# Kernel tuning notes

Hardware: AMD Instinct MI355X
Metric: run time of the kernel (lower is better)

The kernel has to match this reference:

```python
import jax, jax.numpy as jnp
import numpy as np

B, N, C = 256, 196, 768
H, HD = 12, 64          # num_heads, head_dim
WS = 14                 # window side, N = WS*WS
EPS = 1e-6


def setup_inputs() -> dict:
    key = jax.random.key(0)
    ks = jax.random.split(key, 7)
    s = 0.02
    return {
        "x": jax.random.normal(ks[0], (B, N, C), jnp.float32),
        "w_qkv": jax.random.normal(ks[1], (C, 3 * C), jnp.float32) * s,
        "pos_enc": jax.random.normal(ks[2], (1, N, C), jnp.float32) * s,
        "dwc_w": jax.random.normal(ks[3], (HD, 1, 5, 5), jnp.float32) * s,
        "dwc_b": jax.random.normal(ks[4], (HD,), jnp.float32) * s,
        "w_proj": jax.random.normal(ks[5], (C, C), jnp.float32) * s,
        "b_proj": jax.random.normal(ks[6], (C,), jnp.float32) * s,
    }


def _heads(t):
    # (B, N, C) -> (B*H, N, HD)   ['b n (h c) -> (b h) n c']
    return t.reshape(B, N, H, HD).transpose(0, 2, 1, 3).reshape(B * H, N, HD)


def reference(x, w_qkv, pos_enc, dwc_w, dwc_b, w_proj, b_proj):
    qkv = (x @ w_qkv).reshape(B, N, 3, C)
    q, k, v = qkv[:, :, 0], qkv[:, :, 1], qkv[:, :, 2]
    k = k + pos_enc
    # ReLU kernel feature map
    q = jax.nn.relu(q)
    k = jax.nn.relu(k)
    q, k, v = _heads(q), _heads(k), _heads(v)          # (BH, N, HD) each, fp32
    # normalizer z_i = 1 / (q_i . sum_j k_j + eps)
    z = 1.0 / (jnp.einsum("bic,bc->bi", q, k.sum(axis=1)) + EPS)
    # kv-first order (i*j*(c+d) > c*d*(i+j) for N=196, HD=64)
    kv = jnp.einsum("bjc,bjd->bcd", k, v)              # (BH, HD, HD)
    out = jnp.einsum("bic,bcd,bi->bid", q, kv, z)      # (BH, N, HD)
    # depthwise conv positional mixing on v
    fm = v.transpose(0, 2, 1).reshape(B * H, HD, WS, WS)  # 'b (w h) c -> b c w h'
    fm = jax.lax.conv_general_dilated(
        fm, dwc_w, window_strides=(1, 1), padding="SAME",
        dimension_numbers=("NCHW", "OIHW", "NCHW"), feature_group_count=HD,
    ) + dwc_b[None, :, None, None]
    fm = fm.reshape(B * H, HD, N).transpose(0, 2, 1)   # 'b c w h -> b (w h) c'
    out = out + fm
    # '(b h) n c -> b n (h c)'
    out = out.reshape(B, H, N, HD).transpose(0, 2, 1, 3).reshape(B, N, C)
    return out @ w_proj + b_proj
```

## Files before the change

kernel.cpp:

```cpp
#include <hip/hip_runtime.h>

typedef _Float16 half8_t __attribute__((ext_vector_type(8)));
typedef _Float16 half4_t __attribute__((ext_vector_type(4)));
typedef _Float16 half2_t __attribute__((ext_vector_type(2)));
typedef float f32x4 __attribute__((ext_vector_type(4)));

#define MFMA16(a, b, c) __builtin_amdgcn_mfma_f32_16x16x32_f16((a), (b), (c), 0, 0, 0)

typedef const unsigned int __attribute__((address_space(1)))* gas_ptr;
typedef unsigned int __attribute__((address_space(3)))* las_ptr;

__device__ __forceinline__ void gload16(const void* g, void* l) {
    __builtin_amdgcn_global_load_lds((gas_ptr)g, (las_ptr)l, 16, 0, 0);
}

__device__ __forceinline__ int xcd_swizzle(int bid, int nwg) {
    int xcd = bid & 7, i = bid >> 3;
    int q = nwg >> 3, r = nwg & 7;
    return (xcd < r ? xcd * (q + 1) : r * (q + 1) + (xcd - r) * q) + i;
}


__global__ void cvt_f2h_kernel(const float* __restrict__ in, _Float16* __restrict__ out, int n4) {
    int stride = gridDim.x * blockDim.x;
    for (int i = blockIdx.x * blockDim.x + threadIdx.x; i < n4; i += stride) {
        f32x4 v = *(const f32x4*)(in + (size_t)4 * i);
        half4_t h;
        h[0] = (_Float16)v[0]; h[1] = (_Float16)v[1];
        h[2] = (_Float16)v[2]; h[3] = (_Float16)v[3];
        *(half4_t*)(out + (size_t)4 * i) = h;
    }
}

__global__ void transpose768_kernel(const float* __restrict__ in, _Float16* __restrict__ out, int ncols) {
    int idx = blockIdx.x * 256 + threadIdx.x;
    int total = ncols * 768;
    if (idx < total) {
        int j = idx / 768;
        int k = idx - j * 768;
        out[idx] = (_Float16)in[(size_t)k * ncols + j];
    }
}


#define STG128(kof)                                                               \
    {                                                                             \
        _Pragma("unroll")                                                         \
        for (int i = 0; i < 4; ++i) {                                             \
            gload16(ArowS + (kof) + i * 24576, As + wave * 512 + i * 2048);       \
            gload16(BrowS + (kof) + i * 24576, Bs + wave * 512 + i * 2048);       \
        }                                                                         \
    }

__device__ __forceinline__ void run_gemm128(const _Float16* __restrict__ A,
                                            const _Float16* __restrict__ Bt,
                                            int mbase, int nbase,
                                            _Float16* As, _Float16* Bs,
                                            f32x4 (&acc)[4][4]) {
    const int tid = threadIdx.x;
    const int lane = tid & 63;
    const int wave = tid >> 6;
    const int wm = (wave >> 1) * 64;
    const int wn = (wave & 1) * 64;
    const int l15 = lane & 15;
    const int l4 = lane >> 4;
    const int rs = l15 & 7;
    const int srow = lane >> 3;
    const int ssl = ((lane & 7) ^ srow) << 3;

    #pragma unroll
    for (int mi = 0; mi < 4; ++mi)
        #pragma unroll
        for (int ni = 0; ni < 4; ++ni)
            acc[mi][ni] = (f32x4){0.f, 0.f, 0.f, 0.f};

    const _Float16* ArowS = A + (size_t)(mbase + wave * 8 + srow) * 768 + ssl;
    const _Float16* BrowS = Bt + (size_t)(nbase + wave * 8 + srow) * 768 + ssl;

    for (int kt = 0; kt < 12; ++kt) {
        STG128(kt * 64)
        __syncthreads();
        #pragma unroll
        for (int h = 0; h < 2; ++h) {
            half8_t a[4], b[4];
            #pragma unroll
            for (int mi = 0; mi < 4; ++mi)
                a[mi] = *(const half8_t*)(As + (wm + mi * 16 + l15) * 64 +
                                          (((h * 4 + l4) ^ rs) << 3));
            #pragma unroll
            for (int ni = 0; ni < 4; ++ni)
                b[ni] = *(const half8_t*)(Bs + (wn + ni * 16 + l15) * 64 +
                                          (((h * 4 + l4) ^ rs) << 3));
            #pragma unroll
            for (int mi = 0; mi < 4; ++mi)
                #pragma unroll
                for (int ni = 0; ni < 4; ++ni)
                    acc[mi][ni] = MFMA16(a[mi], b[ni], acc[mi][ni]);
        }
        __syncthreads();
    }
}

__global__ __launch_bounds__(256, 4) void gemm_qkv_kernel(
    const _Float16* __restrict__ xh, const _Float16* __restrict__ wqkvT,
    const float* __restrict__ pos_enc,
    _Float16* __restrict__ qh, _Float16* __restrict__ khT, _Float16* __restrict__ vhT) {
    __shared__ _Float16 As[8192];
    __shared__ _Float16 Bs[8192];
    int bid = blockIdx.x;
    int xcd = bid & 7, i = bid >> 3;
    int xq = xcd & 3, nhalf = xcd >> 2;
    int mtl = i / 9, ntl = i - mtl * 9;
    int mtile = xq * 98 + mtl;
    int ntile = nhalf * 9 + ntl;
    f32x4 acc[4][4];
    run_gemm128(xh, wqkvT, mtile * 128, ntile * 128, As, Bs, acc);

    const int tid = threadIdx.x;
    const int lane = tid & 63;
    const int wave = tid >> 6;
    const int wm = (wave >> 1) * 64;
    const int wn = (wave & 1) * 64;
    const int l15 = lane & 15;
    const int l4 = lane >> 4;

    const int s = ntile / 6;
    const int cb = (ntile - s * 6) * 128 + wn;

    if (s == 0) {
        #pragma unroll
        for (int mi = 0; mi < 4; ++mi) {
            #pragma unroll
            for (int ni = 0; ni < 4; ++ni) {
                int c = cb + ni * 16 + l15;
                int h = c >> 6, d = c & 63;
                #pragma unroll
                for (int r = 0; r < 4; ++r) {
                    int gr = mtile * 128 + wm + mi * 16 + l4 * 4 + r;
                    int b = gr / 196;
                    int n = gr - b * 196;
                    qh[((size_t)(b * 12 + h) * 196 + n) * 64 + d] =
                        (_Float16)fmaxf(acc[mi][ni][r], 0.f);
                }
            }
        }
    } else {
        _Float16* dstT = (s == 1) ? khT : vhT;
        #pragma unroll
        for (int mi = 0; mi < 4; ++mi) {
            int gr0 = mtile * 128 + wm + mi * 16 + l4 * 4;
            int b = gr0 / 196, n0 = gr0 - b * 196;
            #pragma unroll
            for (int ni = 0; ni < 4; ++ni) {
                int c = cb + ni * 16 + l15;
                int h = c >> 6, d = c & 63;
                _Float16* row = dstT + ((size_t)(b * 12 + h) * 64 + d) * 224;
                half4_t w;
                #pragma unroll
                for (int r = 0; r < 4; ++r) {
                    float v = acc[mi][ni][r];
                    if (s == 1) { v += pos_enc[(n0 + r) * 768 + c]; v = fmaxf(v, 0.f); }
                    w[r] = (_Float16)v;
                }
                *(half4_t*)(row + n0) = w;
                if (n0 == 192) {
                    half4_t z4 = {(_Float16)0.f, (_Float16)0.f, (_Float16)0.f, (_Float16)0.f};
                    #pragma unroll
                    for (int p = 196; p < 224; p += 4) *(half4_t*)(row + p) = z4;
                }
            }
        }
    }
}

__global__ __launch_bounds__(256, 4) void gemm_proj_kernel(
    const _Float16* __restrict__ fused, const _Float16* __restrict__ wprojT,
    const float* __restrict__ b_proj, float* __restrict__ out) {
    __shared__ _Float16 As[8192];
    __shared__ _Float16 Bs[8192];
    int wgid = xcd_swizzle(blockIdx.x, 392 * 6);
    int mtile = wgid / 6, ntile = wgid - mtile * 6;
    f32x4 acc[4][4];
    run_gemm128(fused, wprojT, mtile * 128, ntile * 128, As, Bs, acc);

    const int tid = threadIdx.x;
    const int lane = tid & 63;
    const int wave = tid >> 6;
    const int wm = (wave >> 1) * 64;
    const int wn = (wave & 1) * 64;
    const int l15 = lane & 15;
    const int l4 = lane >> 4;

    #pragma unroll
    for (int mi = 0; mi < 4; ++mi) {
        #pragma unroll
        for (int ni = 0; ni < 4; ++ni) {
            int gc = ntile * 128 + wn + ni * 16 + l15;
            float bp = b_proj[gc];
            #pragma unroll
            for (int r = 0; r < 4; ++r) {
                int gr = mtile * 128 + wm + mi * 16 + l4 * 4 + r;
                out[(size_t)gr * 768 + gc] = acc[mi][ni][r] + bp;
            }
        }
    }
}

__global__ __launch_bounds__(512, 6) void attn_fused_kernel(
    const _Float16* __restrict__ qh, const _Float16* __restrict__ khT,
    const _Float16* __restrict__ vhT,
    const float* __restrict__ dwc_w, const float* __restrict__ dwc_b,
    _Float16* __restrict__ fused) {
    __shared__ _Float16 kv_l[64 * 64];
    __shared__ _Float16 pv[64 * 236];
    __shared__ float ksum[64];
    __shared__ float zz[196];

    int bh = blockIdx.x;
    int bb = bh / 12, hh = bh - bb * 12;
    int tid = threadIdx.x;
    int lane = tid & 63, wave = tid >> 6;
    int l15 = lane & 15, l4 = lane >> 4;
    size_t kbase = (size_t)bh * 14336;
    size_t qbase = (size_t)bh * 12544;

    #pragma unroll
    for (int j = 0; j < 8; ++j) {
        int c = wave * 8 + j;
        float s = 0.f;
        if (lane < 49) {
            half4_t kq = *(const half4_t*)(khT + kbase + c * 224 + lane * 4);
            s = (float)kq[0] + (float)kq[1] + (float)kq[2] + (float)kq[3];
        }
        #pragma unroll
        for (int off = 32; off; off >>= 1) s += __shfl_down(s, off);
        if (lane == 0) ksum[c] = s;
    }

    {
        int ct = wave >> 1, dt0 = (wave & 1) * 2;
        const _Float16* ka  = khT + kbase + (ct * 16 + l15) * 224 + l4 * 8;
        const _Float16* vb0 = vhT + kbase + (dt0 * 16 + l15) * 224 + l4 * 8;
        const _Float16* vb1 = vb0 + 16 * 224;
        f32x4 acc0 = {0.f, 0.f, 0.f, 0.f}, acc1 = {0.f, 0.f, 0.f, 0.f};
        #pragma unroll
        for (int ks = 0; ks < 7; ++ks) {
            half8_t a  = *(const half8_t*)(ka + ks * 32);
            half8_t b0 = *(const half8_t*)(vb0 + ks * 32);
            half8_t b1 = *(const half8_t*)(vb1 + ks * 32);
            acc0 = MFMA16(a, b0, acc0);
            acc1 = MFMA16(a, b1, acc1);
        }
        half4_t h0, h1;
        #pragma unroll
        for (int r = 0; r < 4; ++r) { h0[r] = (_Float16)acc0[r]; h1[r] = (_Float16)acc1[r]; }
        int slot = ct * 2 + (l4 >> 1), sub = (l4 & 1) * 4;
        int d0 = dt0 * 16 + l15, d1 = d0 + 16;
        *(half4_t*)(kv_l + d0 * 64 + (((slot ^ (d0 & 7)) << 3) + sub)) = h0;
        *(half4_t*)(kv_l + d1 * 64 + (((slot ^ (d1 & 7)) << 3) + sub)) = h1;
    }
    __syncthreads();

    if (tid < 196) {
        const _Float16* qrow = qh + qbase + tid * 64;
        float s = 0.f;
        #pragma unroll
        for (int c8 = 0; c8 < 8; ++c8) {
            half8_t qv = *(const half8_t*)(qrow + c8 * 8);
            #pragma unroll
            for (int j = 0; j < 8; ++j) s += (float)qv[j] * ksum[c8 * 8 + j];
        }
        zz[tid] = 1.0f / (s + 1e-6f);
    }
    __syncthreads();

    for (int t = wave; t < 52; t += 8) {
        int mt = t >> 2, dt = t & 3;
        int d = dt * 16 + l15;
        f32x4 acc = {0.f, 0.f, 0.f, 0.f};
        const _Float16* qrow = qh + qbase + (mt * 16 + l15) * 64;
        half8_t a0 = *(const half8_t*)(qrow + l4 * 8);
        half8_t a1 = *(const half8_t*)(qrow + 32 + l4 * 8);
        half8_t b0 = *(const half8_t*)(kv_l + d * 64 + ((l4 ^ (d & 7)) << 3));
        half8_t b1 = *(const half8_t*)(kv_l + d * 64 + (((l4 + 4) ^ (d & 7)) << 3));
        acc = MFMA16(a0, b0, acc);
        acc = MFMA16(a1, b1, acc);
        int i0 = mt * 16 + l4 * 4;
        half4_t w;
        #pragma unroll
        for (int r = 0; r < 4; ++r) {
            int i = i0 + r;
            w[r] = (_Float16)(acc[r] * ((i < 196) ? zz[i] : 0.f));
        }
        *(half4_t*)(pv + d * 236 + i0) = w;
    }
    __syncthreads();

    #pragma unroll
    for (int rnd = 0; rnd < 2; ++rnd) {
        int y = rnd * 8 + wave;
        int d = lane;
        if (y < 14) {
            float cacc[14];
            float bd = dwc_b[d];
            #pragma unroll
            for (int x = 0; x < 14; ++x) cacc[x] = bd;
            const float* wrow = dwc_w + d * 25;
            #pragma unroll
            for (int ky = 0; ky < 5; ++ky) {
                int yy = y + ky - 2;
                if ((unsigned)yy < 14u) {
                    const _Float16* vr = vhT + kbase + d * 224 + yy * 14;
                    float hv[14];
                    #pragma unroll
                    for (int u = 0; u < 7; ++u) {
                        half2_t w2 = *(const half2_t*)(vr + u * 2);
                        hv[2 * u] = (float)w2[0];
                        hv[2 * u + 1] = (float)w2[1];
                    }
                    #pragma unroll
                    for (int kx = 0; kx < 5; ++kx) {
                        float wk = wrow[ky * 5 + kx];
                        #pragma unroll
                        for (int x = 0; x < 14; ++x) {
                            int c = x + kx - 2;
                            if (c >= 0 && c < 14) cacc[x] += hv[c] * wk;
                        }
                    }
                }
            }
            int ibase = y * 14;
            _Float16* orow = fused + ((size_t)bb * 196 + ibase) * 768 + hh * 64 + d;
            #pragma unroll
            for (int xp = 0; xp < 7; ++xp) {
                half2_t pw = *(const half2_t*)(pv + d * 236 + ibase + 2 * xp);
                orow[(2 * xp) * 768]     = (_Float16)((float)pw[0] + cacc[2 * xp]);
                orow[(2 * xp + 1) * 768] = (_Float16)((float)pw[1] + cacc[2 * xp + 1]);
            }
        }
    }
}


extern "C" void kernel_launch(void* const* d_in, const int* in_sizes, int n_in,
                              void* d_out, int out_size, void* d_ws, size_t ws_size,
                              hipStream_t stream) {
    const float* x       = (const float*)d_in[0];
    const float* w_qkv   = (const float*)d_in[1];
    const float* pos_enc = (const float*)d_in[2];
    const float* dwc_w   = (const float*)d_in[3];
    const float* dwc_b   = (const float*)d_in[4];
    const float* w_proj  = (const float*)d_in[5];
    const float* b_proj  = (const float*)d_in[6];

    const size_t NEEDED = 340574208;
    if (ws_size < NEEDED) return;

    char* ws = (char*)d_ws;
    _Float16* xh     = (_Float16*)(ws + 0);
    _Float16* fused  = xh;
    _Float16* wqkvT  = (_Float16*)(ws + 77070336);
    _Float16* wprojT = (_Float16*)(ws + 80609280);
    _Float16* qh     = (_Float16*)(ws + 81788928);
    _Float16* khT    = (_Float16*)(ws + 158859264);
    _Float16* vhT    = (_Float16*)(ws + 246939648);

    cvt_f2h_kernel<<<4096, 256, 0, stream>>>(x, xh, 9633792);
    transpose768_kernel<<<(2304 * 768 + 255) / 256, 256, 0, stream>>>(w_qkv, wqkvT, 2304);
    transpose768_kernel<<<(768 * 768 + 255) / 256, 256, 0, stream>>>(w_proj, wprojT, 768);
    gemm_qkv_kernel<<<392 * 18, 256, 0, stream>>>(xh, wqkvT, pos_enc, qh, khT, vhT);
    attn_fused_kernel<<<3072, 512, 0, stream>>>(qh, khT, vhT, dwc_w, dwc_b, fused);
    gemm_proj_kernel<<<392 * 6, 256, 0, stream>>>(fused, wprojT, b_proj, (float*)d_out);
}
```

Baseline: 580.2 us.

## Double-buffer GEMM LDS staging with BK=32 to overlap loads with MFMA

The shared 128x128 GEMM mainloop now uses a K tile of 32 instead of 64 and two LDS buffers. The global-to-LDS loads for the next K tile are issued before computing on the current one, with a single barrier per iteration instead of two, and the swizzle pattern is redone for the narrower rows. The aim is to hide global load latency behind MFMA work in both the QKV and projection GEMMs. In exchange there are twice as many iterations with less MFMA work between barriers. The workspace size check is also lowered.

New measurement: 600.0 us. 3.4% more time.

```diff
diff --git a/kernel.cpp b/kernel.cpp
--- a/kernel.cpp
+++ b/kernel.cpp
@@ -43,19 +43,20 @@
 }
 
 
-#define STG128(kof)                                                               \
+#define STG32(buf, kof)                                                           \
     {                                                                             \
-        _Pragma("unroll")                                                         \
-        for (int i = 0; i < 4; ++i) {                                             \
-            gload16(ArowS + (kof) + i * 24576, As + wave * 512 + i * 2048);       \
-            gload16(BrowS + (kof) + i * 24576, Bs + wave * 512 + i * 2048);       \
-        }                                                                         \
+        _Float16* Ad = lds + (buf) * 8192 + wave * 512;                           \
+        _Float16* Bd = lds + (buf) * 8192 + 4096 + wave * 512;                    \
+        gload16(ArowS + (kof), Ad);                                               \
+        gload16(ArowS + (kof) + 49152, Ad + 2048);                                \
+        gload16(BrowS + (kof), Bd);                                               \
+        gload16(BrowS + (kof) + 49152, Bd + 2048);                                \
     }
 
 __device__ __forceinline__ void run_gemm128(const _Float16* __restrict__ A,
                                             const _Float16* __restrict__ Bt,
                                             int mbase, int nbase,
-                                            _Float16* As, _Float16* Bs,
+                                            _Float16* lds,
                                             f32x4 (&acc)[4][4]) {
     const int tid = threadIdx.x;
     const int lane = tid & 63;
@@ -64,9 +65,8 @@
     const int wn = (wave & 1) * 64;
     const int l15 = lane & 15;
     const int l4 = lane >> 4;
-    const int rs = l15 & 7;
-    const int srow = lane >> 3;
-    const int ssl = ((lane & 7) ^ srow) << 3;
+    const int rsw = (l4 ^ ((l15 >> 1) & 3)) << 3;
+    const int ssw = (((tid & 3) ^ ((tid >> 3) & 3)) << 3);
 
     #pragma unroll
     for (int mi = 0; mi < 4; ++mi)
@@ -74,29 +74,31 @@
         for (int ni = 0; ni < 4; ++ni)
             acc[mi][ni] = (f32x4){0.f, 0.f, 0.f, 0.f};
 
-    const _Float16* ArowS = A + (size_t)(mbase + wave * 8 + srow) * 768 + ssl;
-    const _Float16* BrowS = Bt + (size_t)(nbase + wave * 8 + srow) * 768 + ssl;
-
-    for (int kt = 0; kt < 12; ++kt) {
-        STG128(kt * 64)
-        __syncthreads();
-        #pragma unroll
-        for (int h = 0; h < 2; ++h) {
-            half8_t a[4], b[4];
-            #pragma unroll
-            for (int mi = 0; mi < 4; ++mi)
-                a[mi] = *(const half8_t*)(As + (wm + mi * 16 + l15) * 64 +
-                                          (((h * 4 + l4) ^ rs) << 3));
+    const _Float16* ArowS = A + (size_t)(mbase + (tid >> 2)) * 768 + ssw;
+    const _Float16* BrowS = Bt + (size_t)(nbase + (tid >> 2)) * 768 + ssw;
+
+    STG32(0, 0)
+    __syncthreads();
+
+    #pragma unroll 2
+    for (int kt = 0; kt < 24; ++kt) {
+        const int buf = kt & 1;
+        if (kt < 23) STG32(buf ^ 1, (kt + 1) * 32)
+
+        const _Float16* Ac = lds + buf * 8192;
+        const _Float16* Bc = Ac + 4096;
+        half8_t a[4], b[4];
+        #pragma unroll
+        for (int mi = 0; mi < 4; ++mi)
+            a[mi] = *(const half8_t*)(Ac + (wm + mi * 16 + l15) * 32 + rsw);
+        #pragma unroll
+        for (int ni = 0; ni < 4; ++ni)
+            b[ni] = *(const half8_t*)(Bc + (wn + ni * 16 + l15) * 32 + rsw);
+        #pragma unroll
+        for (int mi = 0; mi < 4; ++mi)
             #pragma unroll
             for (int ni = 0; ni < 4; ++ni)
-                b[ni] = *(const half8_t*)(Bs + (wn + ni * 16 + l15) * 64 +
-                                          (((h * 4 + l4) ^ rs) << 3));
-            #pragma unroll
-            for (int mi = 0; mi < 4; ++mi)
-                #pragma unroll
-                for (int ni = 0; ni < 4; ++ni)
-                    acc[mi][ni] = MFMA16(a[mi], b[ni], acc[mi][ni]);
-        }
+                acc[mi][ni] = MFMA16(a[mi], b[ni], acc[mi][ni]);
         __syncthreads();
     }
 }
@@ -105,8 +107,7 @@
     const _Float16* __restrict__ xh, const _Float16* __restrict__ wqkvT,
     const float* __restrict__ pos_enc,
     _Float16* __restrict__ qh, _Float16* __restrict__ khT, _Float16* __restrict__ vhT) {
-    __shared__ _Float16 As[8192];
-    __shared__ _Float16 Bs[8192];
+    __shared__ _Float16 lds[16384];
     int bid = blockIdx.x;
     int xcd = bid & 7, i = bid >> 3;
     int xq = xcd & 3, nhalf = xcd >> 2;
@@ -114,7 +115,7 @@
     int mtile = xq * 98 + mtl;
     int ntile = nhalf * 9 + ntl;
     f32x4 acc[4][4];
-    run_gemm128(xh, wqkvT, mtile * 128, ntile * 128, As, Bs, acc);
+    run_gemm128(xh, wqkvT, mtile * 128, ntile * 128, lds, acc);
 
     const int tid = threadIdx.x;
     const int lane = tid & 63;
@@ -176,12 +177,11 @@
 __global__ __launch_bounds__(256, 4) void gemm_proj_kernel(
     const _Float16* __restrict__ fused, const _Float16* __restrict__ wprojT,
     const float* __restrict__ b_proj, float* __restrict__ out) {
-    __shared__ _Float16 As[8192];
-    __shared__ _Float16 Bs[8192];
+    __shared__ _Float16 lds[16384];
     int wgid = xcd_swizzle(blockIdx.x, 392 * 6);
     int mtile = wgid / 6, ntile = wgid - mtile * 6;
     f32x4 acc[4][4];
-    run_gemm128(fused, wprojT, mtile * 128, ntile * 128, As, Bs, acc);
+    run_gemm128(fused, wprojT, mtile * 128, ntile * 128, lds, acc);
 
     const int tid = threadIdx.x;
     const int lane = tid & 63;
@@ -353,7 +353,7 @@
     const float* w_proj  = (const float*)d_in[5];
     const float* b_proj  = (const float*)d_in[6];
 
-    const size_t NEEDED = 340574208;
+    const size_t NEEDED = 335020032;
     if (ws_size < NEEDED) return;
 
     char* ws = (char*)d_ws;
```
